# Kernel optimization log

Hardware: AMD Instinct MI355X
Metric: run time of the kernel (lower is better)

Reference implementation:

```python
import jax, jax.numpy as jnp
import numpy as np

EPS = 0.01    # self.epsilon
ALPHA = 0.1   # self.alpha


def setup_inputs() -> dict:
    key = jax.random.key(0)
    ks = jax.random.split(key, 10)
    B = 1048576
    s = 0.1  # small init scale, keeps softplus in its smooth regime
    return {
        "X":      jax.random.normal(ks[0], (B, 2), jnp.float32),
        "W_fcnn": jax.random.normal(ks[1], (2, 2), jnp.float32) * s,
        "W1":     jax.random.normal(ks[2], (60, 2), jnp.float32) * s,
        "b1":     jax.random.normal(ks[3], (60,), jnp.float32) * s,
        "W2":     jax.random.normal(ks[4], (60, 60), jnp.float32) * s,
        "b2":     jax.random.normal(ks[5], (60,), jnp.float32) * s,
        "W3":     jax.random.normal(ks[6], (1, 60), jnp.float32) * s,
        "b3":     jax.random.normal(ks[7], (1,), jnp.float32) * s,
        "Wim2":   jax.random.normal(ks[8], (60, 2), jnp.float32) * s,
        "Wim3":   jax.random.normal(ks[9], (1, 2), jnp.float32) * s,
    }


def reference(X, W_fcnn, W1, b1, W2, b2, W3, b3, Wim2, Wim3):
    sp = jax.nn.softplus

    def icnn(x):  # x: [..., 2] -> [..., 1]
        h1 = sp(x @ W1.T + b1)
        h2 = sp(h1 @ W2.T + b2 + x @ Wim2.T)
        return sp(h2 @ W3.T + b3 + x @ Wim3.T)

    # g(0) is computed under torch.no_grad() -> constant; zeros rows are all
    # identical, so one scalar evaluation suffices.
    g0 = jax.lax.stop_gradient(icnn(jnp.zeros((2,), X.dtype))[0])

    def v_row(x):  # scalar Lyapunov value for one state x: [2]
        g = icnn(x)[0]
        # diagonal(X @ X.T) row i == dot(x_i, x_i)
        return jax.nn.relu(g - g0) + EPS * jnp.dot(x, x)

    f_X = X @ W_fcnn.T                      # [B, 2] FCNN (bias-free)
    V = jax.vmap(v_row)(X)                  # [B]
    # torch.autograd.functional.jacobian (create_graph=False) -> detached;
    # per-row grad since V_i only depends on X_i.
    dV = jax.lax.stop_gradient(jax.vmap(jax.grad(v_row))(X))  # [B, 2]

    # diagonal(dV @ f_X.T) == rowwise dot(dV, f_X)
    stab = jnp.sum(dV * f_X, axis=1) + ALPHA * V              # [B]
    dV_norm = dV / jnp.sum(dV * dV, axis=1, keepdims=True)    # [B, 2]
    f_opt = f_X - dV_norm * jax.nn.relu(stab)[:, None]
    return f_opt
```

## Files before the change

kernel.cpp:

```cpp
#include <hip/hip_runtime.h>

#define EPS   0.01f
#define ALPHA 0.1f
#define H     60

typedef __attribute__((ext_vector_type(8))) short short8;
typedef __attribute__((ext_vector_type(4))) float float4v;
typedef __attribute__((ext_vector_type(4))) unsigned u32x4;
typedef __attribute__((ext_vector_type(2))) unsigned u32x2;

__device__ __forceinline__ float softplusf(float x) {
    float e = __expf(-fabsf(x));
    return fmaxf(x, 0.f) + __logf(1.f + e);
}
__device__ __forceinline__ unsigned bf16_rne(float x) {
    unsigned u = __builtin_bit_cast(unsigned, x);
    return (u + 0x7FFFu + ((u >> 16) & 1u)) >> 16;
}
__device__ __forceinline__ float bf16f(unsigned h) {
    return __builtin_bit_cast(float, h << 16);
}
__device__ __forceinline__ int kmap(int q, int j) { return q * 8 + j; }

#define WS_KT  16
#define WS_NT  272
#define WS_A1  528

__global__ void setup_kernel(const float* __restrict__ W1, const float* __restrict__ b1,
                             const float* __restrict__ W2, const float* __restrict__ b2,
                             const float* __restrict__ W3, const float* __restrict__ b3,
                             const float* __restrict__ Wim2, float* __restrict__ ws) {
    const int tid = threadIdx.x;
    float4*   kt  = (float4*)(ws + WS_KT);
    float4*   nt4 = (float4*)(ws + WS_NT);
    unsigned* A1hi = (unsigned*)(ws + WS_A1);
    unsigned* A1lo = A1hi + 2048;
    unsigned* A2hi = A1lo + 2048;
    unsigned* A2lo = A2hi + 2048;

    if (tid < 64) {
        float4 kv = make_float4(0.f, 0.f, 0.f, 0.f);
        float4 nv = make_float4(0.f, 0.f, 0.f, 0.f);
        if (tid < H) {
            kv.x = W1[2 * tid]; kv.y = W1[2 * tid + 1]; kv.z = b1[tid];
            nv.x = b2[tid]; nv.y = Wim2[2 * tid]; nv.z = Wim2[2 * tid + 1]; nv.w = W3[tid];
        }
        kt[tid] = kv; nt4[tid] = nv;
    }
    for (int idx = tid; idx < 2048; idx += 256) {
        const int frag = idx >> 2, rp = idx & 3;
        const int l = frag & 63, t2 = frag >> 6;
        const int kh = t2 & 1, tile = t2 >> 1;
        const int m  = tile * 16 + (l & 15);
        const int ka = kh * 32 + kmap(l >> 4, rp * 2);
        const int kb = kh * 32 + kmap(l >> 4, rp * 2 + 1);
        {
            float v0 = (ka < H && m < H) ? W2[m * H + ka] : 0.f;
            float v1 = (kb < H && m < H) ? W2[m * H + kb] : 0.f;
            unsigned h0 = bf16_rne(v0), h1 = bf16_rne(v1);
            A1hi[idx] = h0 | (h1 << 16);
            A1lo[idx] = bf16_rne(v0 - bf16f(h0)) | (bf16_rne(v1 - bf16f(h1)) << 16);
        }
        {
            float w0 = (ka < H && m < H) ? W2[ka * H + m] : 0.f;
            float w1 = (kb < H && m < H) ? W2[kb * H + m] : 0.f;
            unsigned h0 = bf16_rne(w0), h1 = bf16_rne(w1);
            A2hi[idx] = h0 | (h1 << 16);
            A2lo[idx] = bf16_rne(w0 - bf16f(h0)) | (bf16_rne(w1 - bf16f(h1)) << 16);
        }
    }
    if (tid == 0) {
        float h1v[H];
        for (int k = 0; k < H; ++k) h1v[k] = softplusf(b1[k]);
        float z3 = b3[0];
        for (int j = 0; j < H; ++j) {
            float acc = b2[j];
            for (int k = 0; k < H; ++k) acc = fmaf(W2[j * H + k], h1v[k], acc);
            z3 = fmaf(W3[j], softplusf(acc), z3);
        }
        ws[0] = softplusf(z3);
    }
}

__global__ __launch_bounds__(256) void fused_kernel(
    const float* __restrict__ X, const float* __restrict__ Wf,
    const float* __restrict__ Wim3, const float* __restrict__ b3,
    const float* __restrict__ ws, float* __restrict__ out, int B)
{
    __shared__ unsigned sA1hi[2048], sA1lo[2048], sA2hi[2048], sA2lo[2048];
    __shared__ char Traw[4][2][2304];

    const int tid  = threadIdx.x;
    const int wid  = tid >> 6, lane = tid & 63;
    const int b    = lane & 15, qd = lane >> 4;
    const int rows0 = blockIdx.x * 256;

    {
        const u32x4* gT = (const u32x4*)(ws + WS_A1);
        u32x4* s0 = (u32x4*)sA1hi; u32x4* s1 = (u32x4*)sA1lo;
        u32x4* s2 = (u32x4*)sA2hi; u32x4* s3 = (u32x4*)sA2lo;
        for (int i = tid; i < 512; i += 256) {
            s0[i] = gT[i];
            s1[i] = gT[512 + i];
            s2[i] = gT[1024 + i];
            s3[i] = gT[1536 + i];
        }
    }
    __syncthreads();

    const float g0  = ws[0];
    const float b3v = b3[0], wi30 = Wim3[0], wi31 = Wim3[1];
    const float wf0 = Wf[0], wf1 = Wf[1], wf2 = Wf[2], wf3 = Wf[3];

    const float4* ktT = (const float4*)(ws + WS_KT);
    const float4* ntT = (const float4*)(ws + WS_NT);

    char* Thi = &Traw[wid][0][0];
    char* Tlo = &Traw[wid][1][0];

    for (int blk = 0; blk < 4; ++blk) {
        asm volatile("" ::: "memory");

        const int rloc = wid * 64 + blk * 16;
        const int row  = rows0 + rloc + b;
        const float2 xv = ((const float2*)X)[row < B ? row : 0];
        const float x0 = xv.x, x1 = xv.y;

        short8 B1hi[2], B1lo[2];
#pragma unroll
        for (int kh = 0; kh < 2; ++kh) {
#pragma unroll
            for (int e = 0; e < 8; ++e) {
                const int k = kh * 32 + 8 * qd + e;
                const float4 kv = ktT[k];
                const float z1 = fmaf(kv.x, x0, fmaf(kv.y, x1, kv.z));
                const float h1 = softplusf(z1);
                const unsigned hi = bf16_rne(h1);
                const unsigned lo = bf16_rne(h1 - bf16f(hi));
                B1hi[kh][e] = (short)hi;
                B1lo[kh][e] = (short)lo;
            }
        }

        float4v acc[4];
#pragma unroll
        for (int jt = 0; jt < 4; ++jt) acc[jt] = (float4v){0.f, 0.f, 0.f, 0.f};
#pragma unroll
        for (int jt = 0; jt < 4; ++jt)
#pragma unroll
            for (int kh = 0; kh < 2; ++kh) {
                const int fi = ((jt * 2 + kh) * 64 + lane) * 4;
                const short8 ahi = __builtin_bit_cast(short8, *(const u32x4*)&sA1hi[fi]);
                const short8 alo = __builtin_bit_cast(short8, *(const u32x4*)&sA1lo[fi]);
                acc[jt] = __builtin_amdgcn_mfma_f32_16x16x32_bf16(ahi, B1hi[kh], acc[jt], 0, 0, 0);
                acc[jt] = __builtin_amdgcn_mfma_f32_16x16x32_bf16(alo, B1hi[kh], acc[jt], 0, 0, 0);
                acc[jt] = __builtin_amdgcn_mfma_f32_16x16x32_bf16(ahi, B1lo[kh], acc[jt], 0, 0, 0);
            }

        float z3p = 0.f, gi0p = 0.f, gi1p = 0.f;
#pragma unroll
        for (int jt = 0; jt < 4; ++jt) {
            float tv[4];
#pragma unroll
            for (int c = 0; c < 4; ++c) {
                const int j = jt * 16 + 4 * qd + c;
                const float4 nv = ntT[j];
                const float z2 = acc[jt][c] + fmaf(nv.y, x0, fmaf(nv.z, x1, nv.x));
                const float h2 = softplusf(z2);
                z3p = fmaf(nv.w, h2, z3p);
                const float tj = nv.w * (1.f - __expf(-h2));
                gi0p = fmaf(tj, nv.y, gi0p);
                gi1p = fmaf(tj, nv.z, gi1p);
                tv[c] = tj;
            }
            unsigned hw0 = bf16_rne(tv[0]), hw1 = bf16_rne(tv[1]);
            unsigned hw2 = bf16_rne(tv[2]), hw3 = bf16_rne(tv[3]);
            u32x2 thw, tlw;
            thw.x = hw0 | (hw1 << 16);
            thw.y = hw2 | (hw3 << 16);
            tlw.x = bf16_rne(tv[0] - bf16f(hw0)) | (bf16_rne(tv[1] - bf16f(hw1)) << 16);
            tlw.y = bf16_rne(tv[2] - bf16f(hw2)) | (bf16_rne(tv[3] - bf16f(hw3)) << 16);
            *(u32x2*)(Thi + b * 144 + jt * 32 + qd * 8) = thw;
            *(u32x2*)(Tlo + b * 144 + jt * 32 + qd * 8) = tlw;
        }

        short8 B2hi[2], B2lo[2];
#pragma unroll
        for (int kh = 0; kh < 2; ++kh) {
            B2hi[kh] = *(const short8*)(Thi + b * 144 + kh * 64 + qd * 16);
            B2lo[kh] = *(const short8*)(Tlo + b * 144 + kh * 64 + qd * 16);
        }

        float4v gacc[4];
#pragma unroll
        for (int t = 0; t < 4; ++t) gacc[t] = (float4v){0.f, 0.f, 0.f, 0.f};
#pragma unroll
        for (int t = 0; t < 4; ++t)
#pragma unroll
            for (int kh = 0; kh < 2; ++kh) {
                const int fi = ((t * 2 + kh) * 64 + lane) * 4;
                const short8 ahi = __builtin_bit_cast(short8, *(const u32x4*)&sA2hi[fi]);
                const short8 alo = __builtin_bit_cast(short8, *(const u32x4*)&sA2lo[fi]);
                gacc[t] = __builtin_amdgcn_mfma_f32_16x16x32_bf16(ahi, B2hi[kh], gacc[t], 0, 0, 0);
                gacc[t] = __builtin_amdgcn_mfma_f32_16x16x32_bf16(alo, B2hi[kh], gacc[t], 0, 0, 0);
                gacc[t] = __builtin_amdgcn_mfma_f32_16x16x32_bf16(ahi, B2lo[kh], gacc[t], 0, 0, 0);
            }

        float q0p = 0.f, q1p = 0.f;
#pragma unroll
        for (int t = 0; t < 4; ++t)
#pragma unroll
            for (int c = 0; c < 4; ++c) {
                const int k2 = t * 16 + 4 * qd + c;
                const float4 kv = ktT[k2];
                const float z1 = fmaf(kv.x, x0, fmaf(kv.y, x1, kv.z));
                const float sg = __fdividef(1.f, 1.f + __expf(-z1));
                const float u1 = gacc[t][c] * sg;
                q0p = fmaf(u1, kv.x, q0p);
                q1p = fmaf(u1, kv.y, q1p);
            }

        z3p  += __shfl_xor(z3p, 16);  z3p  += __shfl_xor(z3p, 32);
        gi0p += __shfl_xor(gi0p, 16); gi0p += __shfl_xor(gi0p, 32);
        gi1p += __shfl_xor(gi1p, 16); gi1p += __shfl_xor(gi1p, 32);
        q0p  += __shfl_xor(q0p, 16);  q0p  += __shfl_xor(q0p, 32);
        q1p  += __shfl_xor(q1p, 16);  q1p  += __shfl_xor(q1p, 32);

        const float z3 = z3p + fmaf(wi30, x0, fmaf(wi31, x1, b3v));
        const float g  = softplusf(z3);
        const float u3 = (g > g0) ? (1.f - __expf(-g)) : 0.f;
        const float dv0 = fmaf(2.f * EPS, x0, u3 * (wi30 + gi0p + q0p));
        const float dv1 = fmaf(2.f * EPS, x1, u3 * (wi31 + gi1p + q1p));
        const float V  = fmaxf(g - g0, 0.f) + EPS * fmaf(x0, x0, x1 * x1);
        const float f0 = fmaf(wf0, x0, wf1 * x1);
        const float f1 = fmaf(wf2, x0, wf3 * x1);
        const float stab = fmaf(ALPHA, V, fmaf(dv0, f0, dv1 * f1));
        const float s = __fdividef(fmaxf(stab, 0.f), fmaf(dv0, dv0, dv1 * dv1));
        if (qd == 0 && row < B)
            ((float2*)out)[row] = make_float2(f0 - dv0 * s, f1 - dv1 * s);
    }
}

__global__ void g0_kernel(const float* __restrict__ W2, const float* __restrict__ b1,
                          const float* __restrict__ b2, const float* __restrict__ W3,
                          const float* __restrict__ b3, float* __restrict__ g0_out) {
    if (threadIdx.x != 0 || blockIdx.x != 0) return;
    float h1[H];
    for (int k = 0; k < H; ++k) h1[k] = softplusf(b1[k]);
    float z3 = b3[0];
    for (int j = 0; j < H; ++j) {
        float acc = b2[j];
        for (int k = 0; k < H; ++k) acc = fmaf(W2[j * H + k], h1[k], acc);
        z3 = fmaf(W3[j], softplusf(acc), z3);
    }
    g0_out[0] = softplusf(z3);
}

__global__ __launch_bounds__(256) void sdnn_mono_kernel(
    const float* __restrict__ X,   const float* __restrict__ Wf,
    const float* __restrict__ W1,  const float* __restrict__ b1,
    const float* __restrict__ W2,  const float* __restrict__ b2,
    const float* __restrict__ W3,  const float* __restrict__ b3,
    const float* __restrict__ Wim2,const float* __restrict__ Wim3,
    const float* __restrict__ g0p, float* __restrict__ out, int B)
{
    const int row = blockIdx.x * 256 + threadIdx.x;
    if (row >= B) return;
    const float2 xv = ((const float2*)X)[row];
    const float x0 = xv.x, x1 = xv.y;
    float h1v[H];
#pragma unroll
    for (int k = 0; k < H; ++k)
        h1v[k] = softplusf(fmaf(W1[2 * k], x0, fmaf(W1[2 * k + 1], x1, b1[k])));
    float G[H];
#pragma unroll
    for (int k = 0; k < H; ++k) G[k] = 0.f;
    const float wi30 = Wim3[0], wi31 = Wim3[1];
    float z3 = fmaf(wi30, x0, fmaf(wi31, x1, b3[0]));
    float gim0 = 0.f, gim1 = 0.f;
    for (int j = 0; j < H; ++j) {
        const float* __restrict__ wrow = &W2[j * H];
        float a0 = 0.f, a1 = 0.f, a2 = 0.f, a3 = 0.f;
#pragma unroll
        for (int k = 0; k < H; k += 4) {
            a0 = fmaf(wrow[k + 0], h1v[k + 0], a0);
            a1 = fmaf(wrow[k + 1], h1v[k + 1], a1);
            a2 = fmaf(wrow[k + 2], h1v[k + 2], a2);
            a3 = fmaf(wrow[k + 3], h1v[k + 3], a3);
        }
        float acc = ((a0 + a1) + (a2 + a3))
                  + fmaf(Wim2[2 * j], x0, fmaf(Wim2[2 * j + 1], x1, b2[j]));
        const float h2  = softplusf(acc);
        const float w3j = W3[j];
        z3 = fmaf(w3j, h2, z3);
        const float tj = w3j * (1.f - __expf(-h2));
        gim0 = fmaf(tj, Wim2[2 * j],     gim0);
        gim1 = fmaf(tj, Wim2[2 * j + 1], gim1);
#pragma unroll
        for (int k = 0; k < H; ++k) G[k] = fmaf(wrow[k], tj, G[k]);
    }
    const float g0 = g0p[0];
    const float g  = softplusf(z3);
    const float u3 = (g > g0) ? (1.f - __expf(-g)) : 0.f;
    float q0 = 0.f, q1 = 0.f;
#pragma unroll
    for (int k = 0; k < H; ++k) {
        const float u1 = G[k] * (1.f - __expf(-h1v[k]));
        q0 = fmaf(u1, W1[2 * k],     q0);
        q1 = fmaf(u1, W1[2 * k + 1], q1);
    }
    const float dV0 = fmaf(2.f * EPS, x0, u3 * (wi30 + gim0 + q0));
    const float dV1 = fmaf(2.f * EPS, x1, u3 * (wi31 + gim1 + q1));
    const float V  = fmaxf(g - g0, 0.f) + EPS * fmaf(x0, x0, x1 * x1);
    const float f0 = fmaf(Wf[0], x0, Wf[1] * x1);
    const float f1 = fmaf(Wf[2], x0, Wf[3] * x1);
    const float stab = fmaf(ALPHA, V, fmaf(dV0, f0, dV1 * f1));
    const float s    = __fdividef(fmaxf(stab, 0.f), fmaf(dV0, dV0, dV1 * dV1));
    float2 o;
    o.x = f0 - dV0 * s;
    o.y = f1 - dV1 * s;
    ((float2*)out)[row] = o;
}

extern "C" void kernel_launch(void* const* d_in, const int* in_sizes, int n_in,
                              void* d_out, int out_size, void* d_ws, size_t ws_size,
                              hipStream_t stream) {
    const float* X    = (const float*)d_in[0];
    const float* Wf   = (const float*)d_in[1];
    const float* W1   = (const float*)d_in[2];
    const float* b1   = (const float*)d_in[3];
    const float* W2   = (const float*)d_in[4];
    const float* b2   = (const float*)d_in[5];
    const float* W3   = (const float*)d_in[6];
    const float* b3   = (const float*)d_in[7];
    const float* Wim2 = (const float*)d_in[8];
    const float* Wim3 = (const float*)d_in[9];
    float* out = (float*)d_out;
    float* wsf = (float*)d_ws;

    const int B = in_sizes[0] / 2;
    const int nwg = (B + 255) / 256;

    if (ws_size >= 8720u * 4u) {
        hipLaunchKernelGGL(setup_kernel, dim3(1), dim3(256), 0, stream,
                           W1, b1, W2, b2, W3, b3, Wim2, wsf);
        hipLaunchKernelGGL(fused_kernel, dim3(nwg), dim3(256), 0, stream,
                           X, Wf, Wim3, b3, wsf, out, B);
    } else {
        hipLaunchKernelGGL(g0_kernel, dim3(1), dim3(64), 0, stream,
                           W2, b1, b2, W3, b3, wsf);
        hipLaunchKernelGGL(sdnn_mono_kernel, dim3(nwg), dim3(256), 0, stream,
                           X, Wf, W1, b1, W2, b2, W3, b3, Wim2, Wim3, wsf, out, B);
    }
}
```

Baseline: 209.8 us.

## Drop low-part split for backward GEMM operand and cache K/N tables in LDS

The backward-pass MFMA now uses only the bf16 high part of the tangent vector, which removes the low-part computation, its LDS store and load, and one of three MFMAs per tile. The per-hidden-unit coefficient tables are also staged once into shared memory rather than read repeatedly from global memory. In exchange, the gradient loses some precision because the tangent is rounded to plain bf16.

```diff
diff --git a/kernel.cpp b/kernel.cpp
--- a/kernel.cpp
+++ b/kernel.cpp
@@ -88,7 +88,8 @@
     const float* __restrict__ ws, float* __restrict__ out, int B)
 {
     __shared__ unsigned sA1hi[2048], sA1lo[2048], sA2hi[2048], sA2lo[2048];
-    __shared__ char Traw[4][2][2304];
+    __shared__ float4 sKT[64], sNT[64];
+    __shared__ char Traw[4][2304];
 
     const int tid  = threadIdx.x;
     const int wid  = tid >> 6, lane = tid & 63;
@@ -105,6 +106,10 @@
             s2[i] = gT[1024 + i];
             s3[i] = gT[1536 + i];
         }
+        if (tid < 64) {
+            sKT[tid] = ((const float4*)(ws + WS_KT))[tid];
+            sNT[tid] = ((const float4*)(ws + WS_NT))[tid];
+        }
     }
     __syncthreads();
 
@@ -112,11 +117,7 @@
     const float b3v = b3[0], wi30 = Wim3[0], wi31 = Wim3[1];
     const float wf0 = Wf[0], wf1 = Wf[1], wf2 = Wf[2], wf3 = Wf[3];
 
-    const float4* ktT = (const float4*)(ws + WS_KT);
-    const float4* ntT = (const float4*)(ws + WS_NT);
-
-    char* Thi = &Traw[wid][0][0];
-    char* Tlo = &Traw[wid][1][0];
+    char* Thi = &Traw[wid][0];
 
     for (int blk = 0; blk < 4; ++blk) {
         asm volatile("" ::: "memory");
@@ -132,7 +133,7 @@
 #pragma unroll
             for (int e = 0; e < 8; ++e) {
                 const int k = kh * 32 + 8 * qd + e;
-                const float4 kv = ktT[k];
+                const float4 kv = sKT[k];
                 const float z1 = fmaf(kv.x, x0, fmaf(kv.y, x1, kv.z));
                 const float h1 = softplusf(z1);
                 const unsigned hi = bf16_rne(h1);
@@ -164,7 +165,7 @@
 #pragma unroll
             for (int c = 0; c < 4; ++c) {
                 const int j = jt * 16 + 4 * qd + c;
-                const float4 nv = ntT[j];
+                const float4 nv = sNT[j];
                 const float z2 = acc[jt][c] + fmaf(nv.y, x0, fmaf(nv.z, x1, nv.x));
                 const float h2 = softplusf(z2);
                 z3p = fmaf(nv.w, h2, z3p);
@@ -173,23 +174,16 @@
                 gi1p = fmaf(tj, nv.z, gi1p);
                 tv[c] = tj;
             }
-            unsigned hw0 = bf16_rne(tv[0]), hw1 = bf16_rne(tv[1]);
-            unsigned hw2 = bf16_rne(tv[2]), hw3 = bf16_rne(tv[3]);
-            u32x2 thw, tlw;
-            thw.x = hw0 | (hw1 << 16);
-            thw.y = hw2 | (hw3 << 16);
-            tlw.x = bf16_rne(tv[0] - bf16f(hw0)) | (bf16_rne(tv[1] - bf16f(hw1)) << 16);
-            tlw.y = bf16_rne(tv[2] - bf16f(hw2)) | (bf16_rne(tv[3] - bf16f(hw3)) << 16);
+            u32x2 thw;
+            thw.x = bf16_rne(tv[0]) | (bf16_rne(tv[1]) << 16);
+            thw.y = bf16_rne(tv[2]) | (bf16_rne(tv[3]) << 16);
             *(u32x2*)(Thi + b * 144 + jt * 32 + qd * 8) = thw;
-            *(u32x2*)(Tlo + b * 144 + jt * 32 + qd * 8) = tlw;
-        }
-
-        short8 B2hi[2], B2lo[2];
-#pragma unroll
-        for (int kh = 0; kh < 2; ++kh) {
+        }
+
+        short8 B2hi[2];
+#pragma unroll
+        for (int kh = 0; kh < 2; ++kh)
             B2hi[kh] = *(const short8*)(Thi + b * 144 + kh * 64 + qd * 16);
-            B2lo[kh] = *(const short8*)(Tlo + b * 144 + kh * 64 + qd * 16);
-        }
 
         float4v gacc[4];
 #pragma unroll
@@ -203,7 +197,6 @@
                 const short8 alo = __builtin_bit_cast(short8, *(const u32x4*)&sA2lo[fi]);
                 gacc[t] = __builtin_amdgcn_mfma_f32_16x16x32_bf16(ahi, B2hi[kh], gacc[t], 0, 0, 0);
                 gacc[t] = __builtin_amdgcn_mfma_f32_16x16x32_bf16(alo, B2hi[kh], gacc[t], 0, 0, 0);
-                gacc[t] = __builtin_amdgcn_mfma_f32_16x16x32_bf16(ahi, B2lo[kh], gacc[t], 0, 0, 0);
             }
 
         float q0p = 0.f, q1p = 0.f;
@@ -212,7 +205,7 @@
 #pragma unroll
             for (int c = 0; c < 4; ++c) {
                 const int k2 = t * 16 + 4 * qd + c;
-                const float4 kv = ktT[k2];
+                const float4 kv = sKT[k2];
                 const float z1 = fmaf(kv.x, x0, fmaf(kv.y, x1, kv.z));
                 const float sg = __fdividef(1.f, 1.f + __expf(-z1));
                 const float u1 = gacc[t][c] * sg;
```

New measurement: 209.1 us. About the same (-0.4%).
